# Kernel tuning notes

Measured on AMD Instinct MI355X. Metric: run time of the kernel, lower is better.

The kernel has to match this reference:

```python
import jax, jax.numpy as jnp
import numpy as np

B, T, E, H, V = 512, 128, 64, 512, 100


def setup_inputs() -> dict:
    key = jax.random.key(0)
    ks = jax.random.split(key, 8)
    s = np.float32(1.0 / np.sqrt(H))
    return {
        "dec_input_batch": jax.random.randint(ks[0], (B, T), 0, V, dtype=jnp.int32),
        "dec_input_lengths": jax.random.randint(ks[1], (B,), 1, T + 1, dtype=jnp.int32),
        "input_state_vectors": jax.random.normal(ks[2], (B, H), jnp.float32),
        "char_embeddings": jax.random.normal(ks[3], (V, E), jnp.float32),
        "W0": jax.random.normal(ks[4], (E + 2 * H, 4 * H), jnp.float32) * s,
        "b0": jnp.zeros((4 * H,), jnp.float32),
        "W1": jax.random.normal(ks[5], (2 * H, 4 * H), jnp.float32) * s,
        "b1": jnp.zeros((4 * H,), jnp.float32),
        "Wp": jax.random.normal(ks[6], (H, V), jnp.float32) * np.float32(1.0 / (H + V)),
        "bp": jnp.zeros((V,), jnp.float32),
    }


def _lstm_cell(x, c, h, W, b):
    # TF BasicLSTMCell: gate order i, j, f, o; forget_bias = 1.0
    g = jnp.concatenate([x, h], axis=-1) @ W + b
    i, j, f, o = jnp.split(g, 4, axis=-1)
    nc = c * jax.nn.sigmoid(f + 1.0) + jax.nn.sigmoid(i) * jnp.tanh(j)
    nh = jnp.tanh(nc) * jax.nn.sigmoid(o)
    return nc, nh


def reference(dec_input_batch, dec_input_lengths, input_state_vectors,
              char_embeddings, W0, b0, W1, b1, Wp, bp):
    # embedding lookup + broadcast-concat of the encoder state to every step
    emb = char_embeddings[dec_input_batch]                                  # [B,T,E]
    st = jnp.broadcast_to(input_state_vectors[:, None, :], (B, T, H))       # [B,T,H]
    x = jnp.concatenate([emb, st], axis=-1)                                 # [B,T,E+H]

    # dynamic_rnn sequence_length semantics: zero output, held state past length
    mask = (jnp.arange(T)[:, None] < dec_input_lengths[None, :])[..., None]  # [T,B,1]
    z = jnp.zeros((B, H), jnp.float32)

    def step(carry, inp):
        c0, h0, c1, h1 = carry
        xt, m = inp
        nc0, nh0 = _lstm_cell(xt, c0, h0, W0, b0)
        nc1, nh1 = _lstm_cell(nh0, c1, h1, W1, b1)
        carry = (jnp.where(m, nc0, c0), jnp.where(m, nh0, h0),
                 jnp.where(m, nc1, c1), jnp.where(m, nh1, h1))
        return carry, jnp.where(m, nh1, 0.0)

    _, outs = jax.lax.scan(step, (z, z, z, z), (x.transpose(1, 0, 2), mask))
    outs = outs.transpose(1, 0, 2)                                          # [B,T,H]
    raw_scores = outs @ Wp + bp                                             # [B,T,V]
    return raw_scores
```

## Files before the change

### kernel.cpp

```cpp
#include <hip/hip_runtime.h>
#include <hip/hip_bf16.h>

#define BB 512
#define TT 128
#define EE 64
#define HH 512
#define VV 100
#define NG 2048
#define NBLK 256

typedef __attribute__((ext_vector_type(8))) short bf16x8;
typedef __attribute__((ext_vector_type(4))) float f32x4;

__device__ __forceinline__ float sigm(float x) { return 1.f / (1.f + expf(-x)); }
__device__ __forceinline__ float bf2f(unsigned short u) {
  return __uint_as_float(((unsigned)u) << 16);
}
__device__ __forceinline__ unsigned short f2bf(float x) {
  unsigned u = __float_as_uint(x);
  return (unsigned short)((u + 0x7fffu + ((u >> 16) & 1u)) >> 16);
}
__device__ __forceinline__ void gl16(void* lds, const void* g) {
  __builtin_amdgcn_global_load_lds((const __attribute__((address_space(1))) void*)g,
                                   (__attribute__((address_space(3))) void*)lds, 16, 0, 0);
}
__device__ __forceinline__ unsigned long long ald64(const unsigned short* p) {
  return __hip_atomic_load((const unsigned long long*)p, __ATOMIC_RELAXED,
                           __HIP_MEMORY_SCOPE_AGENT);
}
__device__ __forceinline__ unsigned ald32(const unsigned short* p) {
  return __hip_atomic_load((const unsigned*)p, __ATOMIC_RELAXED,
                           __HIP_MEMORY_SCOPE_AGENT);
}
__device__ __forceinline__ void ast32(unsigned short* p, unsigned v) {
  __hip_atomic_store((unsigned*)p, v, __ATOMIC_RELAXED, __HIP_MEMORY_SCOPE_AGENT);
}
__device__ __forceinline__ int ald32i(const int* p) {
  return __hip_atomic_load(p, __ATOMIC_RELAXED, __HIP_MEMORY_SCOPE_AGENT);
}
__device__ __forceinline__ void ast32i(int* p, int v) {
  __hip_atomic_store(p, v, __ATOMIC_RELAXED, __HIP_MEMORY_SCOPE_AGENT);
}

__global__ __launch_bounds__(256) void pv_kernel(
    const float* __restrict__ cemb, const float* __restrict__ W0,
    float* __restrict__ Pvocab) {
  int idx = blockIdx.x * 256 + threadIdx.x;
  if (idx >= VV * NG) return;
  int v = idx >> 11, n = idx & (NG - 1);
  float acc = 0.f;
  for (int e = 0; e < EE; e++) acc += cemb[v * EE + e] * W0[e * NG + n];
  Pvocab[idx] = acc;
}

__global__ __launch_bounds__(256) void ps_kernel(
    const float* __restrict__ state, const float* __restrict__ W0,
    const float* __restrict__ b0v, float* __restrict__ Pstate) {
  const int rt = blockIdx.x >> 5;
  const int ct = blockIdx.x & 31;
  const int tid = threadIdx.x;
  const int rg = tid >> 4, cg = tid & 15;
  __shared__ float Slds[64][65];
  __shared__ float Wlds[64][65];
  float acc[4][4];
#pragma unroll
  for (int c = 0; c < 4; c++) {
    float bv = b0v[ct * 64 + cg * 4 + c];
#pragma unroll
    for (int r = 0; r < 4; r++) acc[r][c] = bv;
  }
  for (int kc = 0; kc < HH; kc += 64) {
    __syncthreads();
#pragma unroll
    for (int i = 0; i < 16; i++) {
      int e = tid + 256 * i;
      int r = e >> 6, c = e & 63;
      Slds[r][c] = state[(size_t)(rt * 64 + r) * HH + kc + c];
      Wlds[r][c] = W0[(size_t)(EE + kc + r) * NG + ct * 64 + c];
    }
    __syncthreads();
#pragma unroll 1
    for (int kk = 0; kk < 64; kk++) {
      float sv[4], wv[4];
#pragma unroll
      for (int r = 0; r < 4; r++) sv[r] = Slds[rg * 4 + r][kk];
#pragma unroll
      for (int c = 0; c < 4; c++) wv[c] = Wlds[kk][cg * 4 + c];
#pragma unroll
      for (int r = 0; r < 4; r++)
#pragma unroll
        for (int c = 0; c < 4; c++) acc[r][c] += sv[r] * wv[c];
    }
  }
#pragma unroll
  for (int r = 0; r < 4; r++)
#pragma unroll
    for (int c = 0; c < 4; c++)
      Pstate[(size_t)(rt * 64 + rg * 4 + r) * NG + ct * 64 + cg * 4 + c] = acc[r][c];
}

__global__ __launch_bounds__(256) void wconv_kernel(
    const float* __restrict__ W, int koff, unsigned short* __restrict__ Wf,
    int kcmask, int ctshift) {
  int u = blockIdx.x * 256 + threadIdx.x;
  int j = u & 7;
  int lane = (u >> 3) & 63;
  int g = (u >> 9) & 3;
  int kc = (u >> 11) & kcmask;
  int ct16 = u >> ctshift;
  int q = lane >> 4, c15 = lane & 15;
  int k = kc * 32 + q * 8 + j;
  int col = ct16 * 16 + c15 + g * 512;
  float x = W[(size_t)(koff + k) * NG + col];
  unsigned short hi = f2bf(x);
  unsigned short lo = f2bf(x - bf2f(hi));
  size_t base = ((size_t)(ct16 * (kcmask + 1) + kc)) * 4096 + g * 512 + lane * 8 + j;
  Wf[base] = hi;
  Wf[base + 2048] = lo;
}

__global__ __launch_bounds__(256) void wconvp_kernel(
    const float* __restrict__ Wp, unsigned short* __restrict__ Wpf) {
  int u = blockIdx.x * 256 + threadIdx.x;
  int j = u & 7;
  int lane = (u >> 3) & 63;
  int ni = (u >> 9) & 7;
  int kc = (u >> 12) & 15;
  int q = lane >> 4, c15 = lane & 15;
  int col = ni * 16 + c15;
  int k = kc * 32 + q * 8 + j;
  float x = (col < VV) ? Wp[(size_t)k * VV + col] : 0.f;
  unsigned short hi = f2bf(x);
  unsigned short lo = f2bf(x - bf2f(hi));
  size_t base = (size_t)kc * 8192 + ni * 512 + lane * 8 + j;
  Wpf[base] = hi;
  Wpf[base + 4096] = lo;
}

__device__ __forceinline__ void groupbar(unsigned* ctr, unsigned target) {
  __syncthreads();
  if (threadIdx.x == 0) {
    __hip_atomic_fetch_add(ctr, 1u, __ATOMIC_RELAXED, __HIP_MEMORY_SCOPE_AGENT);
    while (__hip_atomic_load(ctr, __ATOMIC_RELAXED, __HIP_MEMORY_SCOPE_AGENT) < target)
      __builtin_amdgcn_s_sleep(1);
  }
  __builtin_amdgcn_sched_barrier(0);
  __syncthreads();
}

__device__ __forceinline__ void ldsbar() {
  asm volatile("s_waitcnt lgkmcnt(0)" ::: "memory");
  __builtin_amdgcn_sched_barrier(0);
  __builtin_amdgcn_s_barrier();
  __builtin_amdgcn_sched_barrier(0);
}

__global__ __launch_bounds__(512, 1) void fused_kernel(
    const int* __restrict__ tok, const int* __restrict__ lens,
    const float* __restrict__ Pstate, const float* __restrict__ Pvocab,
    const unsigned short* __restrict__ W0f, const unsigned short* __restrict__ W1f,
    const float* __restrict__ b1,
    unsigned short* __restrict__ h0f, unsigned short* __restrict__ h1f,
    float* __restrict__ c0, float* __restrict__ c1,
    unsigned short* __restrict__ outsF, unsigned int* __restrict__ bar,
    int* __restrict__ slots) {
  const int bid = blockIdx.x;
  const int tid = threadIdx.x;
  const int wg = (tid >> 6) & 3;
  const int wn = tid >> 8;
  const int lane = tid & 63, c15 = lane & 15, q = lane >> 4;

  __shared__ __align__(16) unsigned short ldsA[2][2048];
  __shared__ float xch[2][32][132];
  __shared__ int s_slots[NBLK];
  __shared__ int s_tile;

  if (tid == 0) {
    unsigned xcd;
    asm volatile("s_getreg_b32 %0, hwreg(HW_REG_XCC_ID, 0, 32)" : "=s"(xcd));
    ast32i(&slots[bid], (int)(xcd & 7));
  }
  groupbar(bar, NBLK);
  if (tid < NBLK) s_slots[tid] = ald32i(&slots[tid]) & 7;
  __syncthreads();
  if (tid == 0) {
    int myx = s_slots[bid];
    int n[8] = {0, 0, 0, 0, 0, 0, 0, 0};
    int rank = 0;
    for (int i = 0; i < NBLK; i++) {
      int v = s_slots[i];
      if (v == myx && i < bid) rank++;
      n[v]++;
    }
    int tile;
    if (rank < 32) {
      tile = myx * 32 + rank;
    } else {
      int o = rank - 32;
      for (int x2 = 0; x2 < myx; x2++) o += (n[x2] > 32) ? (n[x2] - 32) : 0;
      tile = 0;
      for (int x2 = 0; x2 < 8; x2++) {
        int d = 32 - n[x2];
        if (d > 0) {
          if (o < d) { tile = x2 * 32 + n[x2] + o; break; }
          o -= d;
        }
      }
    }
    s_tile = tile;
  }
  __syncthreads();
  const int tile = s_tile;
  const int ct2 = 2 * (tile >> 5) + (tile & 1);
  const int mb = (tile & 31) >> 1;

  const size_t hchunk = (size_t)(mb >> 1) * 16;
  const int mfbase = (mb & 1) * 2;
  unsigned* gctr = bar + 64 + (size_t)mb * 64;

  const int w_hl = tid >> 8;
  const int w_mf = (tid >> 7) & 1;
  const int w_r = tid & 127;
  const size_t a_src = (size_t)w_hl * 2048 + (size_t)(mfbase + w_mf) * 512 + w_r * 4;
  const int a_lds = w_hl * 1024 + w_mf * 512 + w_r * 4;

  const unsigned short* w0base = W0f + ((size_t)(2 * ct2 + wn) * 16) * 4096 + wg * 512 + lane * 8;
  const unsigned short* w1base = W1f + ((size_t)(2 * ct2 + wn) * 32) * 4096 + wg * 512 + lane * 8;

  for (int p = 0; p <= TT; p++) {
    const int wrb = p & 1, rdb = wrb ^ 1;
    const unsigned short* h0r = h0f + (size_t)rdb * 524288;
    const unsigned short* h1r = h1f + (size_t)rdb * 524288;
    unsigned short* h0w = h0f + (size_t)wrb * 524288;
    unsigned short* h1w = h1f + (size_t)wrb * 524288;
    const bool do0 = (p < TT), do1 = (p >= 1);
    const int t0 = p, t1 = p - 1;

    f32x4 acc0[2], acc1[2];
    if (do0) {
#pragma unroll
      for (int mf = 0; mf < 2; mf++)
#pragma unroll
        for (int i = 0; i < 4; i++) {
          int row = mb * 32 + mf * 16 + q * 4 + i;
          int tk = tok[row * TT + t0];
          int col = ct2 * 32 + wn * 16 + c15 + wg * 512;
          acc0[mf][i] = Pstate[(size_t)row * NG + col] + Pvocab[(size_t)tk * NG + col];
        }
    }
    if (do1) {
      float bv = b1[ct2 * 32 + wn * 16 + c15 + wg * 512];
#pragma unroll
      for (int mf = 0; mf < 2; mf++)
#pragma unroll
        for (int i = 0; i < 4; i++) acc1[mf][i] = bv;
    }

    auto aload = [&](int kc) -> unsigned long long {
      const unsigned short* hb = (kc < 16) ? h0r : h1r;
      return ald64(hb + (hchunk + (kc & 15)) * 4096 + a_src);
    };
    auto dswr = [&](int sb, unsigned long long v) {
      *(unsigned long long*)&ldsA[sb][a_lds] = v;
    };
    auto mmac = [&](int sb, bool w0on, bf16x8 B0h, bf16x8 B0l, bf16x8 B1h, bf16x8 B1l) {
      bf16x8 ahi0 = *(const bf16x8*)&ldsA[sb][lane * 8];
      bf16x8 ahi1 = *(const bf16x8*)&ldsA[sb][512 + lane * 8];
      bf16x8 alo0 = *(const bf16x8*)&ldsA[sb][1024 + lane * 8];
      bf16x8 alo1 = *(const bf16x8*)&ldsA[sb][1536 + lane * 8];
      if (w0on) {
        acc0[0] = __builtin_amdgcn_mfma_f32_16x16x32_bf16(ahi0, B0h, acc0[0], 0, 0, 0);
        acc0[0] = __builtin_amdgcn_mfma_f32_16x16x32_bf16(ahi0, B0l, acc0[0], 0, 0, 0);
        acc0[0] = __builtin_amdgcn_mfma_f32_16x16x32_bf16(alo0, B0h, acc0[0], 0, 0, 0);
        acc0[1] = __builtin_amdgcn_mfma_f32_16x16x32_bf16(ahi1, B0h, acc0[1], 0, 0, 0);
        acc0[1] = __builtin_amdgcn_mfma_f32_16x16x32_bf16(ahi1, B0l, acc0[1], 0, 0, 0);
        acc0[1] = __builtin_amdgcn_mfma_f32_16x16x32_bf16(alo1, B0h, acc0[1], 0, 0, 0);
      }
      if (do1) {
        acc1[0] = __builtin_amdgcn_mfma_f32_16x16x32_bf16(ahi0, B1h, acc1[0], 0, 0, 0);
        acc1[0] = __builtin_amdgcn_mfma_f32_16x16x32_bf16(ahi0, B1l, acc1[0], 0, 0, 0);
        acc1[0] = __builtin_amdgcn_mfma_f32_16x16x32_bf16(alo0, B1h, acc1[0], 0, 0, 0);
        acc1[1] = __builtin_amdgcn_mfma_f32_16x16x32_bf16(ahi1, B1h, acc1[1], 0, 0, 0);
        acc1[1] = __builtin_amdgcn_mfma_f32_16x16x32_bf16(ahi1, B1l, acc1[1], 0, 0, 0);
        acc1[1] = __builtin_amdgcn_mfma_f32_16x16x32_bf16(alo1, B1h, acc1[1], 0, 0, 0);
      }
    };

    const int R = do1 ? 32 : 16;

    bf16x8 Ba0h = {}, Ba0l = {}, Ba1h = {}, Ba1l = {};
    bf16x8 Bb0h = {}, Bb0l = {}, Bb1h = {}, Bb1l = {};
    bf16x8 Bc0h = {}, Bc0l = {}, Bc1h = {}, Bc1l = {};
    bf16x8 Bd0h = {}, Bd0l = {}, Bd1h = {}, Bd1l = {};
    if (do0) {
      Ba0h = *(const bf16x8*)(w0base);
      Ba0l = *(const bf16x8*)(w0base + 2048);
      Bb0h = *(const bf16x8*)(w0base + 4096);
      Bb0l = *(const bf16x8*)(w0base + 4096 + 2048);
    }
    if (do1) {
      Ba1h = *(const bf16x8*)(w1base);
      Ba1l = *(const bf16x8*)(w1base + 2048);
      Bb1h = *(const bf16x8*)(w1base + 4096);
      Bb1l = *(const bf16x8*)(w1base + 4096 + 2048);
    }
    unsigned long long a0 = aload(0);
    unsigned long long aN1 = aload(1);
    unsigned long long aN2 = aload(2);
    dswr(0, a0);
    ldsbar();

#pragma unroll 1
    for (int kc = 0; kc < R; kc += 2) {
      unsigned long long aF0 = aload(kc + 3);
      unsigned long long aF1 = aload(kc + 4);
      if (do0 && kc + 2 < 16) {
        const unsigned short* s = w0base + (size_t)(kc + 2) * 4096;
        Bc0h = *(const bf16x8*)(s);
        Bc0l = *(const bf16x8*)(s + 2048);
      }
      if (do1 && kc + 2 < R) {
        const unsigned short* s = w1base + (size_t)(kc + 2) * 4096;
        Bc1h = *(const bf16x8*)(s);
        Bc1l = *(const bf16x8*)(s + 2048);
      }
      if (do0 && kc + 3 < 16) {
        const unsigned short* s = w0base + (size_t)(kc + 3) * 4096;
        Bd0h = *(const bf16x8*)(s);
        Bd0l = *(const bf16x8*)(s + 2048);
      }
      if (do1 && kc + 3 < R) {
        const unsigned short* s = w1base + (size_t)(kc + 3) * 4096;
        Bd1h = *(const bf16x8*)(s);
        Bd1l = *(const bf16x8*)(s + 2048);
      }
      dswr(1, aN1);
      mmac(0, do0 && kc < 16, Ba0h, Ba0l, Ba1h, Ba1l);
      ldsbar();
      dswr(0, aN2);
      mmac(1, do0 && kc + 1 < 16, Bb0h, Bb0l, Bb1h, Bb1l);
      ldsbar();
      aN1 = aF0; aN2 = aF1;
      Ba0h = Bc0h; Ba0l = Bc0l; Ba1h = Bc1h; Ba1l = Bc1l;
      Bb0h = Bd0h; Bb0l = Bd0l; Bb1h = Bd1h; Bb1l = Bd1l;
    }

    if (do0) {
#pragma unroll
      for (int mf = 0; mf < 2; mf++)
#pragma unroll
        for (int i = 0; i < 4; i++)
          xch[0][mf * 16 + q * 4 + i][wg * 32 + wn * 16 + c15] = acc0[mf][i];
    }
    if (do1) {
#pragma unroll
      for (int mf = 0; mf < 2; mf++)
#pragma unroll
        for (int i = 0; i < 4; i++)
          xch[1][mf * 16 + q * 4 + i][wg * 32 + wn * 16 + c15] = acc1[mf][i];
    }
    __syncthreads();
    {
      int rr = tid >> 4, cc = (tid & 15) * 2;
      int row = mb * 32 + rr;
      int cell = ct2 * 32 + cc;
      int qp = cc >> 3, jp = cc & 7;
      size_t hb = (hchunk + ct2) * 4096 + (size_t)(mfbase + (rr >> 4)) * 512 +
                  (size_t)((rr & 15) | (qp << 4)) * 8 + jp;
      int len = lens[row];
      if (do0) {
        bool msk = t0 < len;
        unsigned hhp, hlp;
        if (msk) {
          float gi0 = xch[0][rr][cc], gj0 = xch[0][rr][32 + cc];
          float gf0 = xch[0][rr][64 + cc], go0 = xch[0][rr][96 + cc];
          float gi1 = xch[0][rr][cc + 1], gj1 = xch[0][rr][33 + cc];
          float gf1 = xch[0][rr][65 + cc], go1 = xch[0][rr][97 + cc];
          size_t sidx = (size_t)row * HH + cell;
          float nca = c0[sidx] * sigm(gf0 + 1.f) + sigm(gi0) * tanhf(gj0);
          float ncb = c0[sidx + 1] * sigm(gf1 + 1.f) + sigm(gi1) * tanhf(gj1);
          float nha = tanhf(nca) * sigm(go0);
          float nhb = tanhf(ncb) * sigm(go1);
          c0[sidx] = nca; c0[sidx + 1] = ncb;
          unsigned short ha = f2bf(nha), hbq = f2bf(nhb);
          unsigned short la = f2bf(nha - bf2f(ha)), lb = f2bf(nhb - bf2f(hbq));
          hhp = ha | ((unsigned)hbq << 16);
          hlp = la | ((unsigned)lb << 16);
        } else {
          hhp = ald32(h0r + hb);
          hlp = ald32(h0r + hb + 2048);
        }
        ast32(h0w + hb, hhp);
        ast32(h0w + hb + 2048, hlp);
      }
      if (do1) {
        bool msk = t1 < len;
        unsigned hhp, hlp;
        if (msk) {
          float gi0 = xch[1][rr][cc], gj0 = xch[1][rr][32 + cc];
          float gf0 = xch[1][rr][64 + cc], go0 = xch[1][rr][96 + cc];
          float gi1 = xch[1][rr][cc + 1], gj1 = xch[1][rr][33 + cc];
          float gf1 = xch[1][rr][65 + cc], go1 = xch[1][rr][97 + cc];
          size_t sidx = (size_t)row * HH + cell;
          float nca = c1[sidx] * sigm(gf0 + 1.f) + sigm(gi0) * tanhf(gj0);
          float ncb = c1[sidx + 1] * sigm(gf1 + 1.f) + sigm(gi1) * tanhf(gj1);
          float nha = tanhf(nca) * sigm(go0);
          float nhb = tanhf(ncb) * sigm(go1);
          c1[sidx] = nca; c1[sidx + 1] = ncb;
          unsigned short ha = f2bf(nha), hbq = f2bf(nhb);
          unsigned short la = f2bf(nha - bf2f(ha)), lb = f2bf(nhb - bf2f(hbq));
          hhp = ha | ((unsigned)hbq << 16);
          hlp = la | ((unsigned)lb << 16);
        } else {
          hhp = ald32(h1r + hb);
          hlp = ald32(h1r + hb + 2048);
        }
        ast32(h1w + hb, hhp);
        ast32(h1w + hb + 2048, hlp);
        unsigned op = msk ? hhp : 0u;
        size_t oidx = ((size_t)row * 2 + (t1 >> 6)) * 32768 + (size_t)ct2 * 2048 +
                      (size_t)((t1 >> 4) & 3) * 512 +
                      (size_t)((t1 & 15) | (qp << 4)) * 8 + jp;
        *(unsigned*)&outsF[oidx] = op;
      }
    }

    if (p == TT) break;
    groupbar(gctr, 16u * (unsigned)(p + 1));
  }
}

__global__ __launch_bounds__(128) void proj_kernel(
    const unsigned short* __restrict__ outsF, const unsigned short* __restrict__ Wpf,
    const float* __restrict__ bp, float* __restrict__ out) {
  const int btile = blockIdx.x;
  const int tid = threadIdx.x;
  const int wN = tid >> 6;
  const int lane = tid & 63;
  const int c15 = lane & 15, q = lane >> 4;

  __shared__ __align__(16) unsigned short ldsA[2 * 2048];
  __shared__ __align__(16) unsigned short ldsB2[2 * 8192];

  f32x4 acc[4][4];
#pragma unroll
  for (int m = 0; m < 4; m++)
#pragma unroll
    for (int g = 0; g < 4; g++)
#pragma unroll
      for (int i = 0; i < 4; i++) acc[m][g][i] = 0.f;

  const unsigned short* asrcb = outsF + (size_t)btile * 32768;

  auto stageK = [&](int kc, int buf) {
#pragma unroll
    for (int i2 = 0; i2 < 8; i2++) {
      int f = wN * 8 + i2;
      gl16(&ldsB2[buf * 8192 + f * 512 + lane * 8],
           Wpf + (size_t)kc * 8192 + f * 512 + lane * 8);
    }
#pragma unroll
    for (int i2 = 0; i2 < 2; i2++) {
      int f = wN * 2 + i2;
      gl16(&ldsA[buf * 2048 + f * 512 + lane * 8],
           asrcb + (size_t)kc * 2048 + f * 512 + lane * 8);
    }
  };

  stageK(0, 0);
  __syncthreads();
  for (int kc = 0; kc < 16; kc++) {
    const int buf = kc & 1;
    if (kc + 1 < 16) stageK(kc + 1, buf ^ 1);
    bf16x8 a[4];
#pragma unroll
    for (int m = 0; m < 4; m++)
      a[m] = *(const bf16x8*)&ldsA[buf * 2048 + m * 512 + lane * 8];
#pragma unroll
    for (int g = 0; g < 4; g++) {
      int ni = wN * 4 + g;
      bf16x8 bhi = *(const bf16x8*)&ldsB2[buf * 8192 + ni * 512 + lane * 8];
      bf16x8 blo = *(const bf16x8*)&ldsB2[buf * 8192 + 4096 + ni * 512 + lane * 8];
#pragma unroll
      for (int m = 0; m < 4; m++) {
        acc[m][g] = __builtin_amdgcn_mfma_f32_16x16x32_bf16(a[m], bhi, acc[m][g], 0, 0, 0);
        acc[m][g] = __builtin_amdgcn_mfma_f32_16x16x32_bf16(a[m], blo, acc[m][g], 0, 0, 0);
      }
    }
    __syncthreads();
  }

#pragma unroll
  for (int g = 0; g < 4; g++) {
    int col = (wN * 4 + g) * 16 + c15;
    if (col < VV) {
      float bpv = bp[col];
#pragma unroll
      for (int m = 0; m < 4; m++)
#pragma unroll
        for (int i = 0; i < 4; i++) {
          int rowBT = btile * 64 + m * 16 + q * 4 + i;
          out[(size_t)rowBT * VV + col] = acc[m][g][i] + bpv;
        }
    }
  }
}

extern "C" void kernel_launch(void* const* d_in, const int* in_sizes, int n_in,
                              void* d_out, int out_size, void* d_ws, size_t ws_size,
                              hipStream_t stream) {
  const int* tok = (const int*)d_in[0];
  const int* lens = (const int*)d_in[1];
  const float* state = (const float*)d_in[2];
  const float* cemb = (const float*)d_in[3];
  const float* W0 = (const float*)d_in[4];
  const float* b0 = (const float*)d_in[5];
  const float* W1 = (const float*)d_in[6];
  const float* b1 = (const float*)d_in[7];
  const float* Wp = (const float*)d_in[8];
  const float* bp = (const float*)d_in[9];
  float* out = (float*)d_out;

  char* wsp = (char*)d_ws;
  float* Pstate = (float*)wsp; wsp += (size_t)BB * NG * 4;
  float* Pvocab = (float*)wsp; wsp += (size_t)VV * NG * 4;
  unsigned short* W0f = (unsigned short*)wsp; wsp += (size_t)32 * 16 * 4096 * 2;
  unsigned short* W1f = (unsigned short*)wsp; wsp += (size_t)32 * 32 * 4096 * 2;
  unsigned short* Wpf = (unsigned short*)wsp; wsp += (size_t)16 * 8192 * 2;
  unsigned short* h0f = (unsigned short*)wsp; wsp += (size_t)2 * 524288 * 2;
  unsigned short* h1f = (unsigned short*)wsp; wsp += (size_t)2 * 524288 * 2;
  float* c0 = (float*)wsp; wsp += (size_t)BB * HH * 4;
  float* c1 = (float*)wsp; wsp += (size_t)BB * HH * 4;
  unsigned int* bar = (unsigned int*)wsp; wsp += 8192;
  int* slots = (int*)wsp; wsp += 1024;
  unsigned short* outsF = (unsigned short*)wsp;

  hipMemsetAsync(h0f, 0, (size_t)6 * 1048576 + 8192 + 1024, stream);

  pv_kernel<<<(VV * NG + 255) / 256, 256, 0, stream>>>(cemb, W0, Pvocab);
  ps_kernel<<<256, 256, 0, stream>>>(state, W0, b0, Pstate);
  wconv_kernel<<<4096, 256, 0, stream>>>(W0, EE + HH, W0f, 15, 15);
  wconv_kernel<<<8192, 256, 0, stream>>>(W1, 0, W1f, 31, 16);
  wconvp_kernel<<<(16 * 4096) / 256, 256, 0, stream>>>(Wp, Wpf);

  fused_kernel<<<NBLK, 512, 0, stream>>>(tok, lens, Pstate, Pvocab, W0f, W1f, b1,
                                         h0f, h1f, c0, c1, outsF, bar, slots);

  proj_kernel<<<BB * TT / 64, 128, 0, stream>>>(outsF, Wpf, bp, out);
}
```

Before: 3.036 ms.

## Stage full A operand in LDS once per step and prefetch weights before barrier

The per-step recurrent GEMM now loads all 32 K-chunks of the hidden state into a 128KB shared buffer in one pass. This replaces the double-buffered two-slot LDS pipeline and its per-chunk barriers with a single syncthreads. The first three weight fragments and the gate pre-activations are issued before the inter-block group barrier, which is moved to the top of the step so those global loads overlap the wait. The weight registers become a 4-deep rotating prefetch ring. The cost is much larger LDS use, which is aliased with the gate-exchange buffer, plus extra syncthreads to make that aliasing safe.

```diff
diff --git a/kernel.cpp b/kernel.cpp
--- a/kernel.cpp
+++ b/kernel.cpp
@@ -148,13 +148,6 @@
   __syncthreads();
 }
 
-__device__ __forceinline__ void ldsbar() {
-  asm volatile("s_waitcnt lgkmcnt(0)" ::: "memory");
-  __builtin_amdgcn_sched_barrier(0);
-  __builtin_amdgcn_s_barrier();
-  __builtin_amdgcn_sched_barrier(0);
-}
-
 __global__ __launch_bounds__(512, 1) void fused_kernel(
     const int* __restrict__ tok, const int* __restrict__ lens,
     const float* __restrict__ Pstate, const float* __restrict__ Pvocab,
@@ -170,10 +163,11 @@
   const int wn = tid >> 8;
   const int lane = tid & 63, c15 = lane & 15, q = lane >> 4;
 
-  __shared__ __align__(16) unsigned short ldsA[2][2048];
-  __shared__ float xch[2][32][132];
-  __shared__ int s_slots[NBLK];
-  __shared__ int s_tile;
+  __shared__ __align__(16) unsigned char smem[32 * 4096 + 1024 + 16];
+  unsigned short* ldsA = (unsigned short*)smem;
+  float* xch = (float*)smem;
+  int* s_slots = (int*)(smem + 131072);
+  int* s_tile_p = (int*)(smem + 131072 + 1024);
 
   if (tid == 0) {
     unsigned xcd;
@@ -207,12 +201,13 @@
         }
       }
     }
-    s_tile = tile;
+    *s_tile_p = tile;
   }
   __syncthreads();
-  const int tile = s_tile;
+  const int tile = *s_tile_p;
   const int ct2 = 2 * (tile >> 5) + (tile & 1);
   const int mb = (tile & 31) >> 1;
+  __syncthreads();
 
   const size_t hchunk = (size_t)(mb >> 1) * 16;
   const int mfbase = (mb & 1) * 2;
@@ -235,7 +230,22 @@
     unsigned short* h1w = h1f + (size_t)wrb * 524288;
     const bool do0 = (p < TT), do1 = (p >= 1);
     const int t0 = p, t1 = p - 1;
-
+    const int R = do1 ? 32 : 16;
+
+    bf16x8 B0h[4], B0l[4], B1h[4], B1l[4];
+#pragma unroll
+    for (int s = 0; s < 3; s++) {
+      if (do0) {
+        const unsigned short* sp = w0base + (size_t)s * 4096;
+        B0h[s] = *(const bf16x8*)(sp);
+        B0l[s] = *(const bf16x8*)(sp + 2048);
+      }
+      if (do1) {
+        const unsigned short* sp = w1base + (size_t)s * 4096;
+        B1h[s] = *(const bf16x8*)(sp);
+        B1l[s] = *(const bf16x8*)(sp + 2048);
+      }
+    }
     f32x4 acc0[2], acc1[2];
     if (do0) {
 #pragma unroll
@@ -256,108 +266,69 @@
         for (int i = 0; i < 4; i++) acc1[mf][i] = bv;
     }
 
-    auto aload = [&](int kc) -> unsigned long long {
-      const unsigned short* hb = (kc < 16) ? h0r : h1r;
-      return ald64(hb + (hchunk + (kc & 15)) * 4096 + a_src);
-    };
-    auto dswr = [&](int sb, unsigned long long v) {
-      *(unsigned long long*)&ldsA[sb][a_lds] = v;
-    };
-    auto mmac = [&](int sb, bool w0on, bf16x8 B0h, bf16x8 B0l, bf16x8 B1h, bf16x8 B1l) {
-      bf16x8 ahi0 = *(const bf16x8*)&ldsA[sb][lane * 8];
-      bf16x8 ahi1 = *(const bf16x8*)&ldsA[sb][512 + lane * 8];
-      bf16x8 alo0 = *(const bf16x8*)&ldsA[sb][1024 + lane * 8];
-      bf16x8 alo1 = *(const bf16x8*)&ldsA[sb][1536 + lane * 8];
-      if (w0on) {
-        acc0[0] = __builtin_amdgcn_mfma_f32_16x16x32_bf16(ahi0, B0h, acc0[0], 0, 0, 0);
-        acc0[0] = __builtin_amdgcn_mfma_f32_16x16x32_bf16(ahi0, B0l, acc0[0], 0, 0, 0);
-        acc0[0] = __builtin_amdgcn_mfma_f32_16x16x32_bf16(alo0, B0h, acc0[0], 0, 0, 0);
-        acc0[1] = __builtin_amdgcn_mfma_f32_16x16x32_bf16(ahi1, B0h, acc0[1], 0, 0, 0);
-        acc0[1] = __builtin_amdgcn_mfma_f32_16x16x32_bf16(ahi1, B0l, acc0[1], 0, 0, 0);
-        acc0[1] = __builtin_amdgcn_mfma_f32_16x16x32_bf16(alo1, B0h, acc0[1], 0, 0, 0);
+    if (p > 0) groupbar(gctr, 16u * (unsigned)p);
+
+#pragma unroll
+    for (int i = 0; i < 32; i++) {
+      if (i < R) {
+        const unsigned short* hb = (i < 16) ? h0r : h1r;
+        unsigned long long v = ald64(hb + (hchunk + (i & 15)) * 4096 + a_src);
+        *(unsigned long long*)&ldsA[i * 2048 + a_lds] = v;
+      }
+    }
+    __syncthreads();
+
+#pragma unroll 4
+    for (int kc = 0; kc < R; kc++) {
+      const int sl = kc & 3;
+      const int pf = (kc + 3) & 3;
+      if (do0 && kc + 3 < 16) {
+        const unsigned short* sp = w0base + (size_t)(kc + 3) * 4096;
+        B0h[pf] = *(const bf16x8*)(sp);
+        B0l[pf] = *(const bf16x8*)(sp + 2048);
+      }
+      if (do1 && kc + 3 < R) {
+        const unsigned short* sp = w1base + (size_t)(kc + 3) * 4096;
+        B1h[pf] = *(const bf16x8*)(sp);
+        B1l[pf] = *(const bf16x8*)(sp + 2048);
+      }
+      bf16x8 ahi0 = *(const bf16x8*)&ldsA[kc * 2048 + lane * 8];
+      bf16x8 ahi1 = *(const bf16x8*)&ldsA[kc * 2048 + 512 + lane * 8];
+      bf16x8 alo0 = *(const bf16x8*)&ldsA[kc * 2048 + 1024 + lane * 8];
+      bf16x8 alo1 = *(const bf16x8*)&ldsA[kc * 2048 + 1536 + lane * 8];
+      if (do0 && kc < 16) {
+        acc0[0] = __builtin_amdgcn_mfma_f32_16x16x32_bf16(ahi0, B0h[sl], acc0[0], 0, 0, 0);
+        acc0[0] = __builtin_amdgcn_mfma_f32_16x16x32_bf16(ahi0, B0l[sl], acc0[0], 0, 0, 0);
+        acc0[0] = __builtin_amdgcn_mfma_f32_16x16x32_bf16(alo0, B0h[sl], acc0[0], 0, 0, 0);
+        acc0[1] = __builtin_amdgcn_mfma_f32_16x16x32_bf16(ahi1, B0h[sl], acc0[1], 0, 0, 0);
+        acc0[1] = __builtin_amdgcn_mfma_f32_16x16x32_bf16(ahi1, B0l[sl], acc0[1], 0, 0, 0);
+        acc0[1] = __builtin_amdgcn_mfma_f32_16x16x32_bf16(alo1, B0h[sl], acc0[1], 0, 0, 0);
       }
       if (do1) {
-        acc1[0] = __builtin_amdgcn_mfma_f32_16x16x32_bf16(ahi0, B1h, acc1[0], 0, 0, 0);
-        acc1[0] = __builtin_amdgcn_mfma_f32_16x16x32_bf16(ahi0, B1l, acc1[0], 0, 0, 0);
-        acc1[0] = __builtin_amdgcn_mfma_f32_16x16x32_bf16(alo0, B1h, acc1[0], 0, 0, 0);
-        acc1[1] = __builtin_amdgcn_mfma_f32_16x16x32_bf16(ahi1, B1h, acc1[1], 0, 0, 0);
-        acc1[1] = __builtin_amdgcn_mfma_f32_16x16x32_bf16(ahi1, B1l, acc1[1], 0, 0, 0);
-        acc1[1] = __builtin_amdgcn_mfma_f32_16x16x32_bf16(alo1, B1h, acc1[1], 0, 0, 0);
-      }
-    };
-
-    const int R = do1 ? 32 : 16;
-
-    bf16x8 Ba0h = {}, Ba0l = {}, Ba1h = {}, Ba1l = {};
-    bf16x8 Bb0h = {}, Bb0l = {}, Bb1h = {}, Bb1l = {};
-    bf16x8 Bc0h = {}, Bc0l = {}, Bc1h = {}, Bc1l = {};
-    bf16x8 Bd0h = {}, Bd0l = {}, Bd1h = {}, Bd1l = {};
+        acc1[0] = __builtin_amdgcn_mfma_f32_16x16x32_bf16(ahi0, B1h[sl], acc1[0], 0, 0, 0);
+        acc1[0] = __builtin_amdgcn_mfma_f32_16x16x32_bf16(ahi0, B1l[sl], acc1[0], 0, 0, 0);
+        acc1[0] = __builtin_amdgcn_mfma_f32_16x16x32_bf16(alo0, B1h[sl], acc1[0], 0, 0, 0);
+        acc1[1] = __builtin_amdgcn_mfma_f32_16x16x32_bf16(ahi1, B1h[sl], acc1[1], 0, 0, 0);
+        acc1[1] = __builtin_amdgcn_mfma_f32_16x16x32_bf16(ahi1, B1l[sl], acc1[1], 0, 0, 0);
+        acc1[1] = __builtin_amdgcn_mfma_f32_16x16x32_bf16(alo1, B1h[sl], acc1[1], 0, 0, 0);
+      }
+    }
+
+    __syncthreads();
+
     if (do0) {
-      Ba0h = *(const bf16x8*)(w0base);
-      Ba0l = *(const bf16x8*)(w0base + 2048);
-      Bb0h = *(const bf16x8*)(w0base + 4096);
-      Bb0l = *(const bf16x8*)(w0base + 4096 + 2048);
+#pragma unroll
+      for (int mf = 0; mf < 2; mf++)
+#pragma unroll
+        for (int i = 0; i < 4; i++)
+          xch[(0 * 32 + mf * 16 + q * 4 + i) * 132 + wg * 32 + wn * 16 + c15] = acc0[mf][i];
     }
     if (do1) {
-      Ba1h = *(const bf16x8*)(w1base);
-      Ba1l = *(const bf16x8*)(w1base + 2048);
-      Bb1h = *(const bf16x8*)(w1base + 4096);
-      Bb1l = *(const bf16x8*)(w1base + 4096 + 2048);
-    }
-    unsigned long long a0 = aload(0);
-    unsigned long long aN1 = aload(1);
-    unsigned long long aN2 = aload(2);
-    dswr(0, a0);
-    ldsbar();
-
-#pragma unroll 1
-    for (int kc = 0; kc < R; kc += 2) {
-      unsigned long long aF0 = aload(kc + 3);
-      unsigned long long aF1 = aload(kc + 4);
-      if (do0 && kc + 2 < 16) {
-        const unsigned short* s = w0base + (size_t)(kc + 2) * 4096;
-        Bc0h = *(const bf16x8*)(s);
-        Bc0l = *(const bf16x8*)(s + 2048);
-      }
-      if (do1 && kc + 2 < R) {
-        const unsigned short* s = w1base + (size_t)(kc + 2) * 4096;
-        Bc1h = *(const bf16x8*)(s);
-        Bc1l = *(const bf16x8*)(s + 2048);
-      }
-      if (do0 && kc + 3 < 16) {
-        const unsigned short* s = w0base + (size_t)(kc + 3) * 4096;
-        Bd0h = *(const bf16x8*)(s);
-        Bd0l = *(const bf16x8*)(s + 2048);
-      }
-      if (do1 && kc + 3 < R) {
-        const unsigned short* s = w1base + (size_t)(kc + 3) * 4096;
-        Bd1h = *(const bf16x8*)(s);
-        Bd1l = *(const bf16x8*)(s + 2048);
-      }
-      dswr(1, aN1);
-      mmac(0, do0 && kc < 16, Ba0h, Ba0l, Ba1h, Ba1l);
-      ldsbar();
-      dswr(0, aN2);
-      mmac(1, do0 && kc + 1 < 16, Bb0h, Bb0l, Bb1h, Bb1l);
-      ldsbar();
-      aN1 = aF0; aN2 = aF1;
-      Ba0h = Bc0h; Ba0l = Bc0l; Ba1h = Bc1h; Ba1l = Bc1l;
-      Bb0h = Bd0h; Bb0l = Bd0l; Bb1h = Bd1h; Bb1l = Bd1l;
-    }
-
-    if (do0) {
 #pragma unroll
       for (int mf = 0; mf < 2; mf++)
 #pragma unroll
         for (int i = 0; i < 4; i++)
-          xch[0][mf * 16 + q * 4 + i][wg * 32 + wn * 16 + c15] = acc0[mf][i];
-    }
-    if (do1) {
-#pragma unroll
-      for (int mf = 0; mf < 2; mf++)
-#pragma unroll
-        for (int i = 0; i < 4; i++)
-          xch[1][mf * 16 + q * 4 + i][wg * 32 + wn * 16 + c15] = acc1[mf][i];
+          xch[(1 * 32 + mf * 16 + q * 4 + i) * 132 + wg * 32 + wn * 16 + c15] = acc1[mf][i];
     }
     __syncthreads();
     {
@@ -372,10 +343,9 @@
         bool msk = t0 < len;
         unsigned hhp, hlp;
         if (msk) {
-          float gi0 = xch[0][rr][cc], gj0 = xch[0][rr][32 + cc];
-          float gf0 = xch[0][rr][64 + cc], go0 = xch[0][rr][96 + cc];
-          float gi1 = xch[0][rr][cc + 1], gj1 = xch[0][rr][33 + cc];
-          float gf1 = xch[0][rr][65 + cc], go1 = xch[0][rr][97 + cc];
+          const float* xr = &xch[(0 * 32 + rr) * 132];
+          float gi0 = xr[cc], gj0 = xr[32 + cc], gf0 = xr[64 + cc], go0 = xr[96 + cc];
+          float gi1 = xr[cc + 1], gj1 = xr[33 + cc], gf1 = xr[65 + cc], go1 = xr[97 + cc];
           size_t sidx = (size_t)row * HH + cell;
           float nca = c0[sidx] * sigm(gf0 + 1.f) + sigm(gi0) * tanhf(gj0);
           float ncb = c0[sidx + 1] * sigm(gf1 + 1.f) + sigm(gi1) * tanhf(gj1);
@@ -397,10 +367,9 @@
         bool msk = t1 < len;
         unsigned hhp, hlp;
         if (msk) {
-          float gi0 = xch[1][rr][cc], gj0 = xch[1][rr][32 + cc];
-          float gf0 = xch[1][rr][64 + cc], go0 = xch[1][rr][96 + cc];
-          float gi1 = xch[1][rr][cc + 1], gj1 = xch[1][rr][33 + cc];
-          float gf1 = xch[1][rr][65 + cc], go1 = xch[1][rr][97 + cc];
+          const float* xr = &xch[(1 * 32 + rr) * 132];
+          float gi0 = xr[cc], gj0 = xr[32 + cc], gf0 = xr[64 + cc], go0 = xr[96 + cc];
+          float gi1 = xr[cc + 1], gj1 = xr[33 + cc], gf1 = xr[65 + cc], go1 = xr[97 + cc];
           size_t sidx = (size_t)row * HH + cell;
           float nca = c1[sidx] * sigm(gf0 + 1.f) + sigm(gi0) * tanhf(gj0);
           float ncb = c1[sidx + 1] * sigm(gf1 + 1.f) + sigm(gi1) * tanhf(gj1);
@@ -424,9 +393,6 @@
         *(unsigned*)&outsF[oidx] = op;
       }
     }
-
-    if (p == TT) break;
-    groupbar(gctr, 16u * (unsigned)(p + 1));
   }
 }
 
```

After: 3.566 ms. +17.4%, slower.

## Retile recurrent LSTM kernel to 16-row by 64-cell tiles with earlier weight prefetch

Applied to the files above, without the earlier changes.

Each block now owns 16 batch rows and 64 hidden cells (all 4 gates) instead of 32 rows by 32 cells. Barrier groups shrink from 16 to 8 blocks, and each wave computes two 16-column gate tiles from a single A fragment. Weight fragments are now loaded before the inter-block barrier, which is placed after the accumulator init so global loads overlap the wait. A-operand prefetch depth grows to four chunks and output stores become nontemporal. The cost is more weight traffic per row, since weights are reused across fewer rows, plus more live registers.

```diff
diff --git a/kernel.cpp b/kernel.cpp
--- a/kernel.cpp
+++ b/kernel.cpp
@@ -166,12 +166,13 @@
     int* __restrict__ slots) {
   const int bid = blockIdx.x;
   const int tid = threadIdx.x;
-  const int wg = (tid >> 6) & 3;
-  const int wn = tid >> 8;
+  const int w = tid >> 6;
+  const int g = w >> 1;
+  const int tp = (w & 1) * 2;
   const int lane = tid & 63, c15 = lane & 15, q = lane >> 4;
 
-  __shared__ __align__(16) unsigned short ldsA[2][2048];
-  __shared__ float xch[2][32][132];
+  __shared__ __align__(16) unsigned short ldsA[2][1024];
+  __shared__ float xch2[2][16][272];
   __shared__ int s_slots[NBLK];
   __shared__ int s_tile;
 
@@ -211,21 +212,24 @@
   }
   __syncthreads();
   const int tile = s_tile;
-  const int ct2 = 2 * (tile >> 5) + (tile & 1);
-  const int mb = (tile & 31) >> 1;
-
-  const size_t hchunk = (size_t)(mb >> 1) * 16;
-  const int mfbase = (mb & 1) * 2;
-  unsigned* gctr = bar + 64 + (size_t)mb * 64;
-
-  const int w_hl = tid >> 8;
-  const int w_mf = (tid >> 7) & 1;
-  const int w_r = tid & 127;
-  const size_t a_src = (size_t)w_hl * 2048 + (size_t)(mfbase + w_mf) * 512 + w_r * 4;
-  const int a_lds = w_hl * 1024 + w_mf * 512 + w_r * 4;
-
-  const unsigned short* w0base = W0f + ((size_t)(2 * ct2 + wn) * 16) * 4096 + wg * 512 + lane * 8;
-  const unsigned short* w1base = W1f + ((size_t)(2 * ct2 + wn) * 32) * 4096 + wg * 512 + lane * 8;
+  const int ct2 = tile >> 5;
+  const int mb = tile & 31;
+
+  const size_t hchunkbase = (size_t)(mb >> 2) * 16;
+  const int mf = mb & 3;
+  unsigned* gctr = bar + 64 + mb * 32;
+
+  const bool a_on = tid < 256;
+  const int a_hl = (tid >> 7) & 1;
+  const int a_u = tid & 127;
+  const size_t a_src = (size_t)a_hl * 2048 + (size_t)mf * 512 + a_u * 4;
+  const int a_lds = a_hl * 512 + a_u * 4;
+
+  const int ct16a = ct2 * 4 + tp;
+  const unsigned short* w0a = W0f + (size_t)ct16a * 16 * 4096 + g * 512 + lane * 8;
+  const unsigned short* w0b = w0a + (size_t)16 * 4096;
+  const unsigned short* w1a = W1f + (size_t)ct16a * 32 * 4096 + g * 512 + lane * 8;
+  const unsigned short* w1b = w1a + (size_t)32 * 4096;
 
   for (int p = 0; p <= TT; p++) {
     const int wrb = p & 1, rdb = wrb ^ 1;
@@ -235,148 +239,143 @@
     unsigned short* h1w = h1f + (size_t)wrb * 524288;
     const bool do0 = (p < TT), do1 = (p >= 1);
     const int t0 = p, t1 = p - 1;
+    const int R = do1 ? 32 : 16;
+
+    bf16x8 BregA[8], BregB[8], BregC[8], BregD[8];
+    auto bload = [&](bf16x8* S, int kc) {
+      if (do0 && kc < 16) {
+        const unsigned short* sa = w0a + (size_t)kc * 4096;
+        const unsigned short* sb = w0b + (size_t)kc * 4096;
+        S[0] = *(const bf16x8*)(sa);
+        S[1] = *(const bf16x8*)(sa + 2048);
+        S[2] = *(const bf16x8*)(sb);
+        S[3] = *(const bf16x8*)(sb + 2048);
+      }
+      if (do1 && kc < R) {
+        const unsigned short* sa = w1a + (size_t)kc * 4096;
+        const unsigned short* sb = w1b + (size_t)kc * 4096;
+        S[4] = *(const bf16x8*)(sa);
+        S[5] = *(const bf16x8*)(sa + 2048);
+        S[6] = *(const bf16x8*)(sb);
+        S[7] = *(const bf16x8*)(sb + 2048);
+      }
+    };
+    bload(BregA, 0);
+    bload(BregB, 1);
 
     f32x4 acc0[2], acc1[2];
     if (do0) {
 #pragma unroll
-      for (int mf = 0; mf < 2; mf++)
-#pragma unroll
-        for (int i = 0; i < 4; i++) {
-          int row = mb * 32 + mf * 16 + q * 4 + i;
-          int tk = tok[row * TT + t0];
-          int col = ct2 * 32 + wn * 16 + c15 + wg * 512;
-          acc0[mf][i] = Pstate[(size_t)row * NG + col] + Pvocab[(size_t)tk * NG + col];
+      for (int i = 0; i < 4; i++) {
+        int row = mb * 16 + q * 4 + i;
+        int tk = tok[row * TT + t0];
+        const float* ps = Pstate + (size_t)row * NG;
+        const float* pv = Pvocab + (size_t)tk * NG;
+#pragma unroll
+        for (int s = 0; s < 2; s++) {
+          int col = ct2 * 64 + (tp + s) * 16 + c15 + g * 512;
+          acc0[s][i] = ps[col] + pv[col];
         }
+      }
     }
     if (do1) {
-      float bv = b1[ct2 * 32 + wn * 16 + c15 + wg * 512];
-#pragma unroll
-      for (int mf = 0; mf < 2; mf++)
-#pragma unroll
-        for (int i = 0; i < 4; i++) acc1[mf][i] = bv;
-    }
+#pragma unroll
+      for (int s = 0; s < 2; s++) {
+        float bv = b1[ct2 * 64 + (tp + s) * 16 + c15 + g * 512];
+#pragma unroll
+        for (int i = 0; i < 4; i++) acc1[s][i] = bv;
+      }
+    }
+
+    if (p > 0) groupbar(gctr, 8u * (unsigned)p);
 
     auto aload = [&](int kc) -> unsigned long long {
+      if (!a_on) return 0ull;
       const unsigned short* hb = (kc < 16) ? h0r : h1r;
-      return ald64(hb + (hchunk + (kc & 15)) * 4096 + a_src);
+      return ald64(hb + (hchunkbase + (kc & 15)) * 4096 + a_src);
     };
     auto dswr = [&](int sb, unsigned long long v) {
-      *(unsigned long long*)&ldsA[sb][a_lds] = v;
+      if (a_on) *(unsigned long long*)&ldsA[sb][a_lds] = v;
     };
-    auto mmac = [&](int sb, bool w0on, bf16x8 B0h, bf16x8 B0l, bf16x8 B1h, bf16x8 B1l) {
-      bf16x8 ahi0 = *(const bf16x8*)&ldsA[sb][lane * 8];
-      bf16x8 ahi1 = *(const bf16x8*)&ldsA[sb][512 + lane * 8];
-      bf16x8 alo0 = *(const bf16x8*)&ldsA[sb][1024 + lane * 8];
-      bf16x8 alo1 = *(const bf16x8*)&ldsA[sb][1536 + lane * 8];
-      if (w0on) {
-        acc0[0] = __builtin_amdgcn_mfma_f32_16x16x32_bf16(ahi0, B0h, acc0[0], 0, 0, 0);
-        acc0[0] = __builtin_amdgcn_mfma_f32_16x16x32_bf16(ahi0, B0l, acc0[0], 0, 0, 0);
-        acc0[0] = __builtin_amdgcn_mfma_f32_16x16x32_bf16(alo0, B0h, acc0[0], 0, 0, 0);
-        acc0[1] = __builtin_amdgcn_mfma_f32_16x16x32_bf16(ahi1, B0h, acc0[1], 0, 0, 0);
-        acc0[1] = __builtin_amdgcn_mfma_f32_16x16x32_bf16(ahi1, B0l, acc0[1], 0, 0, 0);
-        acc0[1] = __builtin_amdgcn_mfma_f32_16x16x32_bf16(alo1, B0h, acc0[1], 0, 0, 0);
+    auto mmac = [&](int sb, bool on0, bf16x8* S) {
+      bf16x8 ahi = *(const bf16x8*)&ldsA[sb][lane * 8];
+      bf16x8 alo = *(const bf16x8*)&ldsA[sb][512 + lane * 8];
+      if (on0) {
+        acc0[0] = __builtin_amdgcn_mfma_f32_16x16x32_bf16(ahi, S[0], acc0[0], 0, 0, 0);
+        acc0[0] = __builtin_amdgcn_mfma_f32_16x16x32_bf16(ahi, S[1], acc0[0], 0, 0, 0);
+        acc0[0] = __builtin_amdgcn_mfma_f32_16x16x32_bf16(alo, S[0], acc0[0], 0, 0, 0);
+        acc0[1] = __builtin_amdgcn_mfma_f32_16x16x32_bf16(ahi, S[2], acc0[1], 0, 0, 0);
+        acc0[1] = __builtin_amdgcn_mfma_f32_16x16x32_bf16(ahi, S[3], acc0[1], 0, 0, 0);
+        acc0[1] = __builtin_amdgcn_mfma_f32_16x16x32_bf16(alo, S[2], acc0[1], 0, 0, 0);
       }
       if (do1) {
-        acc1[0] = __builtin_amdgcn_mfma_f32_16x16x32_bf16(ahi0, B1h, acc1[0], 0, 0, 0);
-        acc1[0] = __builtin_amdgcn_mfma_f32_16x16x32_bf16(ahi0, B1l, acc1[0], 0, 0, 0);
-        acc1[0] = __builtin_amdgcn_mfma_f32_16x16x32_bf16(alo0, B1h, acc1[0], 0, 0, 0);
-        acc1[1] = __builtin_amdgcn_mfma_f32_16x16x32_bf16(ahi1, B1h, acc1[1], 0, 0, 0);
-        acc1[1] = __builtin_amdgcn_mfma_f32_16x16x32_bf16(ahi1, B1l, acc1[1], 0, 0, 0);
-        acc1[1] = __builtin_amdgcn_mfma_f32_16x16x32_bf16(alo1, B1h, acc1[1], 0, 0, 0);
+        acc1[0] = __builtin_amdgcn_mfma_f32_16x16x32_bf16(ahi, S[4], acc1[0], 0, 0, 0);
+        acc1[0] = __builtin_amdgcn_mfma_f32_16x16x32_bf16(ahi, S[5], acc1[0], 0, 0, 0);
+        acc1[0] = __builtin_amdgcn_mfma_f32_16x16x32_bf16(alo, S[4], acc1[0], 0, 0, 0);
+        acc1[1] = __builtin_amdgcn_mfma_f32_16x16x32_bf16(ahi, S[6], acc1[1], 0, 0, 0);
+        acc1[1] = __builtin_amdgcn_mfma_f32_16x16x32_bf16(ahi, S[7], acc1[1], 0, 0, 0);
+        acc1[1] = __builtin_amdgcn_mfma_f32_16x16x32_bf16(alo, S[6], acc1[1], 0, 0, 0);
       }
     };
 
-    const int R = do1 ? 32 : 16;
-
-    bf16x8 Ba0h = {}, Ba0l = {}, Ba1h = {}, Ba1l = {};
-    bf16x8 Bb0h = {}, Bb0l = {}, Bb1h = {}, Bb1l = {};
-    bf16x8 Bc0h = {}, Bc0l = {}, Bc1h = {}, Bc1l = {};
-    bf16x8 Bd0h = {}, Bd0l = {}, Bd1h = {}, Bd1l = {};
-    if (do0) {
-      Ba0h = *(const bf16x8*)(w0base);
-      Ba0l = *(const bf16x8*)(w0base + 2048);
-      Bb0h = *(const bf16x8*)(w0base + 4096);
-      Bb0l = *(const bf16x8*)(w0base + 4096 + 2048);
-    }
-    if (do1) {
-      Ba1h = *(const bf16x8*)(w1base);
-      Ba1l = *(const bf16x8*)(w1base + 2048);
-      Bb1h = *(const bf16x8*)(w1base + 4096);
-      Bb1l = *(const bf16x8*)(w1base + 4096 + 2048);
-    }
-    unsigned long long a0 = aload(0);
+    unsigned long long a0v = aload(0);
     unsigned long long aN1 = aload(1);
     unsigned long long aN2 = aload(2);
-    dswr(0, a0);
+    unsigned long long aN3 = aload(3);
+    unsigned long long aN4 = aload(4);
+    dswr(0, a0v);
     ldsbar();
 
 #pragma unroll 1
     for (int kc = 0; kc < R; kc += 2) {
-      unsigned long long aF0 = aload(kc + 3);
-      unsigned long long aF1 = aload(kc + 4);
-      if (do0 && kc + 2 < 16) {
-        const unsigned short* s = w0base + (size_t)(kc + 2) * 4096;
-        Bc0h = *(const bf16x8*)(s);
-        Bc0l = *(const bf16x8*)(s + 2048);
-      }
-      if (do1 && kc + 2 < R) {
-        const unsigned short* s = w1base + (size_t)(kc + 2) * 4096;
-        Bc1h = *(const bf16x8*)(s);
-        Bc1l = *(const bf16x8*)(s + 2048);
-      }
-      if (do0 && kc + 3 < 16) {
-        const unsigned short* s = w0base + (size_t)(kc + 3) * 4096;
-        Bd0h = *(const bf16x8*)(s);
-        Bd0l = *(const bf16x8*)(s + 2048);
-      }
-      if (do1 && kc + 3 < R) {
-        const unsigned short* s = w1base + (size_t)(kc + 3) * 4096;
-        Bd1h = *(const bf16x8*)(s);
-        Bd1l = *(const bf16x8*)(s + 2048);
-      }
+      unsigned long long aF0 = aload(kc + 5);
+      unsigned long long aF1 = aload(kc + 6);
+      bload(BregC, kc + 2);
+      bload(BregD, kc + 3);
       dswr(1, aN1);
-      mmac(0, do0 && kc < 16, Ba0h, Ba0l, Ba1h, Ba1l);
+      mmac(0, do0 && kc < 16, BregA);
       ldsbar();
       dswr(0, aN2);
-      mmac(1, do0 && kc + 1 < 16, Bb0h, Bb0l, Bb1h, Bb1l);
+      mmac(1, do0 && kc + 1 < 16, BregB);
       ldsbar();
-      aN1 = aF0; aN2 = aF1;
-      Ba0h = Bc0h; Ba0l = Bc0l; Ba1h = Bc1h; Ba1l = Bc1l;
-      Bb0h = Bd0h; Bb0l = Bd0l; Bb1h = Bd1h; Bb1l = Bd1l;
+      aN1 = aN3; aN2 = aN4; aN3 = aF0; aN4 = aF1;
+#pragma unroll
+      for (int z = 0; z < 8; z++) { BregA[z] = BregC[z]; BregB[z] = BregD[z]; }
     }
 
     if (do0) {
 #pragma unroll
-      for (int mf = 0; mf < 2; mf++)
+      for (int s = 0; s < 2; s++)
 #pragma unroll
         for (int i = 0; i < 4; i++)
-          xch[0][mf * 16 + q * 4 + i][wg * 32 + wn * 16 + c15] = acc0[mf][i];
+          xch2[0][q * 4 + i][g * 68 + (tp + s) * 16 + c15] = acc0[s][i];
     }
     if (do1) {
 #pragma unroll
-      for (int mf = 0; mf < 2; mf++)
+      for (int s = 0; s < 2; s++)
 #pragma unroll
         for (int i = 0; i < 4; i++)
-          xch[1][mf * 16 + q * 4 + i][wg * 32 + wn * 16 + c15] = acc1[mf][i];
+          xch2[1][q * 4 + i][g * 68 + (tp + s) * 16 + c15] = acc1[s][i];
     }
     __syncthreads();
     {
-      int rr = tid >> 4, cc = (tid & 15) * 2;
-      int row = mb * 32 + rr;
-      int cell = ct2 * 32 + cc;
-      int qp = cc >> 3, jp = cc & 7;
-      size_t hb = (hchunk + ct2) * 4096 + (size_t)(mfbase + (rr >> 4)) * 512 +
-                  (size_t)((rr & 15) | (qp << 4)) * 8 + jp;
+      int rr = tid >> 5, cc = (tid & 31) * 2;
+      int row = mb * 16 + rr;
+      int cellg = ct2 * 64 + cc;
+      int kch = cellg >> 5;
+      int col32 = cellg & 31;
+      int qp = col32 >> 3, jp = col32 & 7;
+      size_t hb = (hchunkbase + kch) * 4096 + (size_t)mf * 512 +
+                  (size_t)(rr | (qp << 4)) * 8 + jp;
       int len = lens[row];
       if (do0) {
         bool msk = t0 < len;
         unsigned hhp, hlp;
         if (msk) {
-          float gi0 = xch[0][rr][cc], gj0 = xch[0][rr][32 + cc];
-          float gf0 = xch[0][rr][64 + cc], go0 = xch[0][rr][96 + cc];
-          float gi1 = xch[0][rr][cc + 1], gj1 = xch[0][rr][33 + cc];
-          float gf1 = xch[0][rr][65 + cc], go1 = xch[0][rr][97 + cc];
-          size_t sidx = (size_t)row * HH + cell;
+          const float* xr = &xch2[0][rr][0];
+          float gi0 = xr[cc], gj0 = xr[68 + cc], gf0 = xr[136 + cc], go0 = xr[204 + cc];
+          float gi1 = xr[cc + 1], gj1 = xr[69 + cc], gf1 = xr[137 + cc], go1 = xr[205 + cc];
+          size_t sidx = (size_t)row * HH + cellg;
           float nca = c0[sidx] * sigm(gf0 + 1.f) + sigm(gi0) * tanhf(gj0);
           float ncb = c0[sidx + 1] * sigm(gf1 + 1.f) + sigm(gi1) * tanhf(gj1);
           float nha = tanhf(nca) * sigm(go0);
@@ -397,11 +396,10 @@
         bool msk = t1 < len;
         unsigned hhp, hlp;
         if (msk) {
-          float gi0 = xch[1][rr][cc], gj0 = xch[1][rr][32 + cc];
-          float gf0 = xch[1][rr][64 + cc], go0 = xch[1][rr][96 + cc];
-          float gi1 = xch[1][rr][cc + 1], gj1 = xch[1][rr][33 + cc];
-          float gf1 = xch[1][rr][65 + cc], go1 = xch[1][rr][97 + cc];
-          size_t sidx = (size_t)row * HH + cell;
+          const float* xr = &xch2[1][rr][0];
+          float gi0 = xr[cc], gj0 = xr[68 + cc], gf0 = xr[136 + cc], go0 = xr[204 + cc];
+          float gi1 = xr[cc + 1], gj1 = xr[69 + cc], gf1 = xr[137 + cc], go1 = xr[205 + cc];
+          size_t sidx = (size_t)row * HH + cellg;
           float nca = c1[sidx] * sigm(gf0 + 1.f) + sigm(gi0) * tanhf(gj0);
           float ncb = c1[sidx + 1] * sigm(gf1 + 1.f) + sigm(gi1) * tanhf(gj1);
           float nha = tanhf(nca) * sigm(go0);
@@ -418,15 +416,12 @@
         ast32(h1w + hb, hhp);
         ast32(h1w + hb + 2048, hlp);
         unsigned op = msk ? hhp : 0u;
-        size_t oidx = ((size_t)row * 2 + (t1 >> 6)) * 32768 + (size_t)ct2 * 2048 +
+        size_t oidx = ((size_t)row * 2 + (t1 >> 6)) * 32768 + (size_t)kch * 2048 +
                       (size_t)((t1 >> 4) & 3) * 512 +
                       (size_t)((t1 & 15) | (qp << 4)) * 8 + jp;
-        *(unsigned*)&outsF[oidx] = op;
-      }
-    }
-
-    if (p == TT) break;
-    groupbar(gctr, 16u * (unsigned)(p + 1));
+        __builtin_nontemporal_store(op, (unsigned*)&outsF[oidx]);
+      }
+    }
   }
 }
 
```

New measurement: 3.576 ms. +17.8%, slower.

## Map batch row-blocks to XCDs and use cache-local h loads when placement is balanced

Applied to the files above, without the earlier changes.

Changes the tile mapping so that each XCD owns whole batch row-blocks, with all column tiles of a row-block on the same die. It also records whether every XCD got exactly 32 blocks. In that balanced case, hidden-state exchange loads and stores use plain volatile accesses instead of the system-coherent atomic-style helpers, so they can be served from the XCD-local L2. This relies on the per-row-block barrier group being confined to one XCD for coherence, and falls back to the old accessors when placement is unbalanced.

```diff
diff --git a/kernel.cpp b/kernel.cpp
--- a/kernel.cpp
+++ b/kernel.cpp
@@ -174,6 +174,7 @@
   __shared__ float xch[2][32][132];
   __shared__ int s_slots[NBLK];
   __shared__ int s_tile;
+  __shared__ int s_fast;
 
   if (tid == 0) {
     unsigned xcd;
@@ -208,15 +209,19 @@
       }
     }
     s_tile = tile;
+    int ok = 1;
+    for (int x2 = 0; x2 < 8; x2++) ok &= (n[x2] == 32);
+    s_fast = ok;
   }
   __syncthreads();
   const int tile = s_tile;
-  const int ct2 = 2 * (tile >> 5) + (tile & 1);
-  const int mb = (tile & 31) >> 1;
+  const bool fastp = (s_fast != 0);
+  const int mb = 2 * (tile >> 5) + ((tile >> 4) & 1);
+  const int ct2 = tile & 15;
 
   const size_t hchunk = (size_t)(mb >> 1) * 16;
   const int mfbase = (mb & 1) * 2;
-  unsigned* gctr = bar + 64 + (size_t)mb * 64;
+  unsigned* gctr = bar + 64 + mb * 64;
 
   const int w_hl = tid >> 8;
   const int w_mf = (tid >> 7) & 1;
@@ -258,17 +263,19 @@
 
     auto aload = [&](int kc) -> unsigned long long {
       const unsigned short* hb = (kc < 16) ? h0r : h1r;
-      return ald64(hb + (hchunk + (kc & 15)) * 4096 + a_src);
+      const unsigned short* pp = hb + (hchunk + (kc & 15)) * 4096 + a_src;
+      if (fastp) return *(volatile const unsigned long long*)pp;
+      return ald64(pp);
     };
     auto dswr = [&](int sb, unsigned long long v) {
       *(unsigned long long*)&ldsA[sb][a_lds] = v;
     };
-    auto mmac = [&](int sb, bool w0on, bf16x8 B0h, bf16x8 B0l, bf16x8 B1h, bf16x8 B1l) {
+    auto mmac = [&](int sb, bool on0, bf16x8 B0h, bf16x8 B0l, bf16x8 B1h, bf16x8 B1l) {
       bf16x8 ahi0 = *(const bf16x8*)&ldsA[sb][lane * 8];
       bf16x8 ahi1 = *(const bf16x8*)&ldsA[sb][512 + lane * 8];
       bf16x8 alo0 = *(const bf16x8*)&ldsA[sb][1024 + lane * 8];
       bf16x8 alo1 = *(const bf16x8*)&ldsA[sb][1536 + lane * 8];
-      if (w0on) {
+      if (on0) {
         acc0[0] = __builtin_amdgcn_mfma_f32_16x16x32_bf16(ahi0, B0h, acc0[0], 0, 0, 0);
         acc0[0] = __builtin_amdgcn_mfma_f32_16x16x32_bf16(ahi0, B0l, acc0[0], 0, 0, 0);
         acc0[0] = __builtin_amdgcn_mfma_f32_16x16x32_bf16(alo0, B0h, acc0[0], 0, 0, 0);
@@ -304,10 +311,10 @@
       Bb1h = *(const bf16x8*)(w1base + 4096);
       Bb1l = *(const bf16x8*)(w1base + 4096 + 2048);
     }
-    unsigned long long a0 = aload(0);
+    unsigned long long a0v = aload(0);
     unsigned long long aN1 = aload(1);
     unsigned long long aN2 = aload(2);
-    dswr(0, a0);
+    dswr(0, a0v);
     ldsbar();
 
 #pragma unroll 1
@@ -387,11 +394,21 @@
           hhp = ha | ((unsigned)hbq << 16);
           hlp = la | ((unsigned)lb << 16);
         } else {
-          hhp = ald32(h0r + hb);
-          hlp = ald32(h0r + hb + 2048);
-        }
-        ast32(h0w + hb, hhp);
-        ast32(h0w + hb + 2048, hlp);
+          if (fastp) {
+            hhp = *(volatile const unsigned*)(h0r + hb);
+            hlp = *(volatile const unsigned*)(h0r + hb + 2048);
+          } else {
+            hhp = ald32(h0r + hb);
+            hlp = ald32(h0r + hb + 2048);
+          }
+        }
+        if (fastp) {
+          *(volatile unsigned*)(h0w + hb) = hhp;
+          *(volatile unsigned*)(h0w + hb + 2048) = hlp;
+        } else {
+          ast32(h0w + hb, hhp);
+          ast32(h0w + hb + 2048, hlp);
+        }
       }
       if (do1) {
         bool msk = t1 < len;
@@ -412,11 +429,21 @@
           hhp = ha | ((unsigned)hbq << 16);
           hlp = la | ((unsigned)lb << 16);
         } else {
-          hhp = ald32(h1r + hb);
-          hlp = ald32(h1r + hb + 2048);
-        }
-        ast32(h1w + hb, hhp);
-        ast32(h1w + hb + 2048, hlp);
+          if (fastp) {
+            hhp = *(volatile const unsigned*)(h1r + hb);
+            hlp = *(volatile const unsigned*)(h1r + hb + 2048);
+          } else {
+            hhp = ald32(h1r + hb);
+            hlp = ald32(h1r + hb + 2048);
+          }
+        }
+        if (fastp) {
+          *(volatile unsigned*)(h1w + hb) = hhp;
+          *(volatile unsigned*)(h1w + hb + 2048) = hlp;
+        } else {
+          ast32(h1w + hb, hhp);
+          ast32(h1w + hb + 2048, hlp);
+        }
         unsigned op = msk ? hhp : 0u;
         size_t oidx = ((size_t)row * 2 + (t1 >> 6)) * 32768 + (size_t)ct2 * 2048 +
                       (size_t)((t1 >> 4) & 3) * 512 +
```

Result: slower. 3.935 ms (+29.6%).
